# Optimization experiments

Hardware: AMD Instinct MI355X
Metric: run time of the kernel (lower is better)

## Reference

```python
import jax, jax.numpy as jnp
import numpy as np

BATCH = 4096
NNZ = 32
VOCAB = 1_000_000
DIM = 64


def setup_inputs() -> dict:
    key = jax.random.key(0)
    k1, k2, k3, k4 = jax.random.split(key, 4)
    idx = jax.random.randint(k1, (BATCH, NNZ), 0, VOCAB, dtype=jnp.int32)
    vals = jax.random.uniform(k2, (BATCH, NNZ), dtype=jnp.float32)
    kernel = jax.random.normal(k3, (VOCAB, DIM), dtype=jnp.float32)
    bias = jax.random.normal(k4, (DIM,), dtype=jnp.float32)
    return {"idx": idx, "vals": vals, "kernel": kernel, "bias": bias}


def reference(idx, vals, kernel, bias):
    # Sparse [B, V] x dense [V, D] matmul == weighted gather-sum (embedding bag)
    gathered = kernel[idx]                      # [B, nnz, D] irregular gather
    out = jnp.einsum("bn,bnd->bd", vals, gathered) + bias  # [B, D]
    return out
```

## Files before the change

### kernel.cpp

```cpp
#include <hip/hip_runtime.h>
#include <hip/hip_bf16.h>


#define B_BATCH 4096
#define NNZ 32
#define DIM 64
#define LANES_PER_ROW 16

__global__ __launch_bounds__(256) void sparse_embed_kernel(
    const int* __restrict__ idx,
    const float* __restrict__ vals,
    const float* __restrict__ kern,
    const float* __restrict__ bias,
    float* __restrict__ out)
{
    const int tid  = blockIdx.x * blockDim.x + threadIdx.x;
    const int row  = tid >> 4;
    const int lane = tid & 15;
    if (row >= B_BATCH) return;

    const int*   irow = idx  + row * NNZ;
    const float* vrow = vals + row * NNZ;

    float4 acc = make_float4(0.f, 0.f, 0.f, 0.f);

    #pragma unroll
    for (int n = 0; n < NNZ; ++n) {
        const int   id = irow[n];
        const float v  = vrow[n];
        const float4 k = *reinterpret_cast<const float4*>(
            kern + (size_t)id * DIM + lane * 4);
        acc.x += v * k.x;
        acc.y += v * k.y;
        acc.z += v * k.z;
        acc.w += v * k.w;
    }

    const float4 b4 = *reinterpret_cast<const float4*>(bias + lane * 4);
    acc.x += b4.x;
    acc.y += b4.y;
    acc.z += b4.z;
    acc.w += b4.w;

    *reinterpret_cast<float4*>(out + (size_t)row * DIM + lane * 4) = acc;
}

extern "C" void kernel_launch(void* const* d_in, const int* in_sizes, int n_in,
                              void* d_out, int out_size, void* d_ws, size_t ws_size,
                              hipStream_t stream) {
    const int*   idx  = (const int*)  d_in[0];
    const float* vals = (const float*)d_in[1];
    const float* kern = (const float*)d_in[2];
    const float* bias = (const float*)d_in[3];
    float* out = (float*)d_out;

    const int threads = 256;
    const int total   = B_BATCH * LANES_PER_ROW;
    const int blocks  = (total + threads - 1) / threads;

    sparse_embed_kernel<<<blocks, threads, 0, stream>>>(idx, vals, kern, bias, out);
}
```

Before: 297.1 us.

## Map one wavefront per row with scalar index loads and preloaded indices

Each 64-lane wavefront now handles one output row, one float per lane, instead of 16 lanes per row with float4 loads. The row index is made wave-uniform with readfirstlane so the index and value loads can become scalar loads, and all 32 indices and weights are loaded up front so the 32 gathers can be issued back to back. This is meant to raise memory-level parallelism and cut per-lane address arithmetic, at the cost of 4x more threads and narrower per-lane loads.

```diff
diff --git a/kernel.cpp b/kernel.cpp
--- a/kernel.cpp
+++ b/kernel.cpp
@@ -5,7 +5,6 @@
 #define B_BATCH 4096
 #define NNZ 32
 #define DIM 64
-#define LANES_PER_ROW 16
 
 __global__ __launch_bounds__(256) void sparse_embed_kernel(
     const int* __restrict__ idx,
@@ -14,35 +13,30 @@
     const float* __restrict__ bias,
     float* __restrict__ out)
 {
-    const int tid  = blockIdx.x * blockDim.x + threadIdx.x;
-    const int row  = tid >> 4;
-    const int lane = tid & 15;
-    if (row >= B_BATCH) return;
+    const int lane = threadIdx.x & 63;
+    int row = (blockIdx.x << 2) + (threadIdx.x >> 6);
+    row = __builtin_amdgcn_readfirstlane(row);
 
     const int*   irow = idx  + row * NNZ;
     const float* vrow = vals + row * NNZ;
 
-    float4 acc = make_float4(0.f, 0.f, 0.f, 0.f);
+    int   ids[NNZ];
+    float vs[NNZ];
+    #pragma unroll
+    for (int n = 0; n < NNZ; ++n) {
+        ids[n] = irow[n];
+        vs[n]  = vrow[n];
+    }
+
+    float acc = bias[lane];
 
     #pragma unroll
     for (int n = 0; n < NNZ; ++n) {
-        const int   id = irow[n];
-        const float v  = vrow[n];
-        const float4 k = *reinterpret_cast<const float4*>(
-            kern + (size_t)id * DIM + lane * 4);
-        acc.x += v * k.x;
-        acc.y += v * k.y;
-        acc.z += v * k.z;
-        acc.w += v * k.w;
+        const float k = kern[(size_t)ids[n] * DIM + lane];
+        acc = fmaf(vs[n], k, acc);
     }
 
-    const float4 b4 = *reinterpret_cast<const float4*>(bias + lane * 4);
-    acc.x += b4.x;
-    acc.y += b4.y;
-    acc.z += b4.z;
-    acc.w += b4.w;
-
-    *reinterpret_cast<float4*>(out + (size_t)row * DIM + lane * 4) = acc;
+    out[row * DIM + lane] = acc;
 }
 
 extern "C" void kernel_launch(void* const* d_in, const int* in_sizes, int n_in,
@@ -55,8 +49,7 @@
     float* out = (float*)d_out;
 
     const int threads = 256;
-    const int total   = B_BATCH * LANES_PER_ROW;
-    const int blocks  = (total + threads - 1) / threads;
+    const int blocks  = B_BATCH / 4;
 
     sparse_embed_kernel<<<blocks, threads, 0, stream>>>(idx, vals, kern, bias, out);
 }
```

After: 297.2 us. No clear change (+0.0%).
